# Kernel tuning notes

Hardware: AMD Instinct MI355X
Metric: run time of the kernel (lower is better)

## Reference

```python
import jax, jax.numpy as jnp
import numpy as np

CHANNELS = 256
LAYERS = 4
IN_FEAT = 118
N_NODES = 20000
N_EDGES = 320000


def setup_inputs() -> dict:
    key = jax.random.key(0)
    ks = jax.random.split(key, 4 + 4 * LAYERS)
    x = jax.random.normal(ks[0], (N_NODES, IN_FEAT), dtype=jnp.float32)
    edge_index = jax.random.randint(ks[1], (2, N_EDGES), 0, N_NODES, dtype=jnp.int64)
    s = 1.0 / np.sqrt(CHANNELS)
    W_embed = jax.random.normal(ks[2], (IN_FEAT, CHANNELS), dtype=jnp.float32) / np.sqrt(IN_FEAT)
    b_embed = jnp.zeros((CHANNELS,), dtype=jnp.float32)
    W1 = jax.random.normal(ks[3], (LAYERS, CHANNELS, CHANNELS), dtype=jnp.float32) * s
    b1 = jnp.zeros((LAYERS, CHANNELS), dtype=jnp.float32)
    W2 = jax.random.normal(ks[4], (LAYERS, CHANNELS, CHANNELS), dtype=jnp.float32) * s
    b2 = jnp.zeros((LAYERS, CHANNELS), dtype=jnp.float32)
    return {"x": x, "edge_index": edge_index, "W_embed": W_embed, "b_embed": b_embed,
            "W1": W1, "b1": b1, "W2": W2, "b2": b2}


def reference(x, edge_index, W_embed, b_embed, W1, b1, W2, b2):
    n = x.shape[0]
    src, dst = edge_index[0], edge_index[1]
    # in-degree for mean aggregation (constant across layers)
    cnt = jax.ops.segment_sum(jnp.ones(src.shape[0], dtype=x.dtype), dst, num_segments=n)
    inv_cnt = (1.0 / jnp.maximum(cnt, 1.0))[:, None]
    h = x @ W_embed + b_embed  # [N, C]
    for l in range(W1.shape[0]):
        # message: gather source features, dense + exact GELU (dropout off in eval)
        msg = jax.nn.gelu(h[src] @ W1[l] + b1[l], approximate=False)  # [E, C]
        # mean-scatter aggregate over destination nodes
        agg = jax.ops.segment_sum(msg, dst, num_segments=n) * inv_cnt  # [N, C]
        # update: dense + GELU
        h = jax.nn.gelu(agg @ W2[l] + b2[l], approximate=False)
    return jnp.mean(h, axis=1)  # [N]
```

## Files before the change

### kernel.cpp

```cpp
#include <hip/hip_runtime.h>
#include <math.h>

#define CH 256

typedef _Float16 half8 __attribute__((ext_vector_type(8)));
typedef _Float16 half4 __attribute__((ext_vector_type(4)));
typedef float f32x4 __attribute__((ext_vector_type(4)));

__device__ __forceinline__ float gelu_exact(float v) {
    return 0.5f * v * (1.0f + erff(v * 0.70710678118654752f));
}

__global__ void wsplit_kernel(const float* __restrict__ W1, const float* __restrict__ W2,
                              _Float16* __restrict__ WThi, _Float16* __restrict__ WTlo) {
    int idx = blockIdx.x * blockDim.x + threadIdx.x;
    int n   = idx & 255;
    int kg  = (idx >> 8) & 31;
    int mat = idx >> 13;
    const float* W = (mat < 4) ? (W1 + (size_t)mat * 65536)
                               : (W2 + (size_t)(mat - 4) * 65536);
    _Float16 hi[8], lo[8];
#pragma unroll
    for (int j = 0; j < 8; j++) {
        float v = W[(size_t)(kg * 8 + j) * CH + n];
        _Float16 h = (_Float16)v;
        hi[j] = h;
        lo[j] = (_Float16)(v - (float)h);
    }
    size_t off = (size_t)mat * 65536 + (size_t)n * 256 + kg * 8;
    *(half8*)(WThi + off) = *(half8*)&hi[0];
    *(half8*)(WTlo + off) = *(half8*)&lo[0];
}

__global__ void wesplit_kernel(const float* __restrict__ We,
                               _Float16* __restrict__ WeTh, _Float16* __restrict__ WeTl) {
    int idx = blockIdx.x * blockDim.x + threadIdx.x;
    if (idx >= 4096) return;
    int n  = idx >> 4;
    int k8 = (idx & 15) * 8;
    _Float16 hi[8], lo[8];
#pragma unroll
    for (int j = 0; j < 8; j++) {
        int k = k8 + j;
        float v = (k < 118) ? We[(size_t)k * CH + n] : 0.f;
        _Float16 h = (_Float16)v;
        hi[j] = h;
        lo[j] = (_Float16)(v - (float)h);
    }
    size_t off = (size_t)n * 128 + k8;
    *(half8*)(WeTh + off) = *(half8*)&hi[0];
    *(half8*)(WeTl + off) = *(half8*)&lo[0];
}

__global__ void xsplit_kernel(const float* __restrict__ x,
                              _Float16* __restrict__ xh, _Float16* __restrict__ xl, int N) {
    int idx = blockIdx.x * blockDim.x + threadIdx.x;
    int n  = idx >> 4;
    int c8 = (idx & 15) * 8;
    if (n >= N) return;
    _Float16 hi[8], lo[8];
#pragma unroll
    for (int j = 0; j < 8; j++) {
        int c = c8 + j;
        float v = (c < 118) ? x[(size_t)n * 118 + c] : 0.f;
        _Float16 h = (_Float16)v;
        hi[j] = h;
        lo[j] = (_Float16)(v - (float)h);
    }
    size_t off = (size_t)n * 128 + c8;
    *(half8*)(xh + off) = *(half8*)&hi[0];
    *(half8*)(xl + off) = *(half8*)&lo[0];
}

template<int KT, bool DOGELU>
__global__ __launch_bounds__(256, 4) void mgemm_kernel(
    const _Float16* __restrict__ Ah_g, const _Float16* __restrict__ Al_g,
    const _Float16* __restrict__ Bh_g, const _Float16* __restrict__ Bl_g,
    const float* __restrict__ bias,
    _Float16* __restrict__ Oh, _Float16* __restrict__ Ol,
    int M)
{
    const int KLEN = KT * 32;
    __shared__ _Float16 Ah[128][40], Al[128][40], Bh[64][40], Bl[64][40];

    int tid  = threadIdx.x;
    int lane = tid & 63;
    int wave = tid >> 6;
    int wr = wave >> 1;
    int wc = wave & 1;
    int m0 = blockIdx.x * 128;
    int n0 = blockIdx.y * 64;

    f32x4 acc[4][2];
#pragma unroll
    for (int i = 0; i < 4; i++)
#pragma unroll
        for (int j = 0; j < 2; j++) acc[i][j] = (f32x4){0.f, 0.f, 0.f, 0.f};

    const int s_row = tid >> 1;
    const int s_ch  = (tid & 1) * 16;
    const size_t s_arow = (size_t)min(m0 + s_row, M - 1);
    const int bcol = (tid & 127) >> 1;
    const int bch  = (tid & 1) * 16;

    for (int kt = 0; kt < KT; kt++) {
        int k0 = kt * 32;
        {
            const _Float16* sh_ = Ah_g + s_arow * KLEN + k0 + s_ch;
            const _Float16* sl_ = Al_g + s_arow * KLEN + k0 + s_ch;
            half8 h0 = ((const half8*)sh_)[0];
            half8 h1 = ((const half8*)sh_)[1];
            half8 l0 = ((const half8*)sl_)[0];
            half8 l1 = ((const half8*)sl_)[1];
            *(half8*)&Ah[s_row][s_ch]     = h0;
            *(half8*)&Ah[s_row][s_ch + 8] = h1;
            *(half8*)&Al[s_row][s_ch]     = l0;
            *(half8*)&Al[s_row][s_ch + 8] = l1;
        }
        {
            const _Float16* bs = ((tid < 128) ? Bh_g : Bl_g)
                                 + (size_t)(n0 + bcol) * KLEN + k0 + bch;
            half8 u0 = ((const half8*)bs)[0];
            half8 u1 = ((const half8*)bs)[1];
            _Float16 (*dst)[40] = (tid < 128) ? Bh : Bl;
            *(half8*)&dst[bcol][bch]     = u0;
            *(half8*)&dst[bcol][bch + 8] = u1;
        }
        __syncthreads();

        {
            int frow = lane & 15;
            int fk   = (lane >> 4) * 8;
            half8 ah[4], al[4], bh[2], bl[2];
#pragma unroll
            for (int rf = 0; rf < 4; rf++) {
                int r = wr * 64 + rf * 16 + frow;
                ah[rf] = *(const half8*)&Ah[r][fk];
                al[rf] = *(const half8*)&Al[r][fk];
            }
#pragma unroll
            for (int cf = 0; cf < 2; cf++) {
                int c = wc * 32 + cf * 16 + frow;
                bh[cf] = *(const half8*)&Bh[c][fk];
                bl[cf] = *(const half8*)&Bl[c][fk];
            }
#pragma unroll
            for (int rf = 0; rf < 4; rf++)
#pragma unroll
                for (int cf = 0; cf < 2; cf++) {
                    acc[rf][cf] = __builtin_amdgcn_mfma_f32_16x16x32_f16(ah[rf], bh[cf], acc[rf][cf], 0, 0, 0);
                    acc[rf][cf] = __builtin_amdgcn_mfma_f32_16x16x32_f16(ah[rf], bl[cf], acc[rf][cf], 0, 0, 0);
                    acc[rf][cf] = __builtin_amdgcn_mfma_f32_16x16x32_f16(al[rf], bh[cf], acc[rf][cf], 0, 0, 0);
                }
        }
        __syncthreads();
    }

    int ccol = lane & 15;
    int crow = (lane >> 4) * 4;
#pragma unroll
    for (int cf = 0; cf < 2; cf++) {
        int gcol = n0 + wc * 32 + cf * 16 + ccol;
        float bb = bias[gcol];
#pragma unroll
        for (int rf = 0; rf < 4; rf++) {
#pragma unroll
            for (int q = 0; q < 4; q++) {
                int grow = m0 + wr * 64 + rf * 16 + crow + q;
                if (grow < M) {
                    float v = acc[rf][cf][q] + bb;
                    float g = DOGELU ? gelu_exact(v) : v;
                    _Float16 hi = (_Float16)g;
                    Oh[(size_t)grow * CH + gcol] = hi;
                    Ol[(size_t)grow * CH + gcol] = (_Float16)(g - (float)hi);
                }
            }
        }
    }
}

__global__ void zero_int_kernel(int* p, int n) {
    int i = blockIdx.x * blockDim.x + threadIdx.x;
    if (i < n) p[i] = 0;
}

__global__ void degree_kernel(const int* __restrict__ ei, int E, int* deg) {
    int e = blockIdx.x * blockDim.x + threadIdx.x;
    if (e < E) atomicAdd(&deg[ei[E + e]], 1);
}

__global__ void scan_part_kernel(const int* __restrict__ deg, int* bsum, int N) {
    int t = threadIdx.x;
    int base = blockIdx.x * 1024 + t * 4;
    int4 v = {0, 0, 0, 0};
    if (base + 3 < N) v = *(const int4*)(deg + base);
    else {
        if (base + 0 < N) v.x = deg[base + 0];
        if (base + 1 < N) v.y = deg[base + 1];
        if (base + 2 < N) v.z = deg[base + 2];
        if (base + 3 < N) v.w = deg[base + 3];
    }
    __shared__ int sh[256];
    sh[t] = v.x + v.y + v.z + v.w;
    __syncthreads();
    for (int off = 128; off; off >>= 1) {
        if (t < off) sh[t] += sh[t + off];
        __syncthreads();
    }
    if (t == 0) bsum[blockIdx.x] = sh[0];
}

__global__ void scan_top_kernel(const int* __restrict__ bsum, int* boff, int B) {
    __shared__ int sh[256];
    int t = threadIdx.x;
    int own = (t < B) ? bsum[t] : 0;
    sh[t] = own;
    __syncthreads();
    for (int off = 1; off < 256; off <<= 1) {
        int v = (t >= off) ? sh[t - off] : 0;
        __syncthreads();
        sh[t] += v;
        __syncthreads();
    }
    if (t < B) boff[t] = sh[t] - own;
}

__global__ void scan_final_kernel(const int* __restrict__ deg, const int* __restrict__ boff,
                                  int* row_ptr, int* fill_pos, float* inv, int N, int E) {
    int t = threadIdx.x;
    int base = blockIdx.x * 1024 + t * 4;
    int4 v = {0, 0, 0, 0};
    if (base + 3 < N) v = *(const int4*)(deg + base);
    else {
        if (base + 0 < N) v.x = deg[base + 0];
        if (base + 1 < N) v.y = deg[base + 1];
        if (base + 2 < N) v.z = deg[base + 2];
        if (base + 3 < N) v.w = deg[base + 3];
    }
    int own = v.x + v.y + v.z + v.w;
    __shared__ int sh[256];
    sh[t] = own;
    __syncthreads();
    for (int off = 1; off < 256; off <<= 1) {
        int s = (t >= off) ? sh[t - off] : 0;
        __syncthreads();
        sh[t] += s;
        __syncthreads();
    }
    int run = boff[blockIdx.x] + (sh[t] - own);
    int4 rp;
    rp.x = run;
    rp.y = run + v.x;
    rp.z = rp.y + v.y;
    rp.w = rp.z + v.z;
    if (base + 3 < N) {
        *(int4*)(row_ptr + base) = rp;
        *(int4*)(fill_pos + base) = rp;
        float4 iv;
        iv.x = 1.0f / fmaxf((float)v.x, 1.0f);
        iv.y = 1.0f / fmaxf((float)v.y, 1.0f);
        iv.z = 1.0f / fmaxf((float)v.z, 1.0f);
        iv.w = 1.0f / fmaxf((float)v.w, 1.0f);
        *(float4*)(inv + base) = iv;
    } else {
        int rr[4] = {rp.x, rp.y, rp.z, rp.w};
        int dd[4] = {v.x, v.y, v.z, v.w};
        for (int q = 0; q < 4; q++) {
            if (base + q < N) {
                row_ptr[base + q] = rr[q];
                fill_pos[base + q] = rr[q];
                inv[base + q] = 1.0f / fmaxf((float)dd[q], 1.0f);
            }
        }
    }
    if (blockIdx.x == 0 && t == 0) row_ptr[N] = E;
}

__global__ void fill_kernel(const int* __restrict__ ei, int E, int* fill_pos, int* colv) {
    int e = blockIdx.x * blockDim.x + threadIdx.x;
    if (e < E) {
        int p = atomicAdd(&fill_pos[ei[E + e]], 1);
        colv[p] = ei[e];
    }
}

__global__ void agg_kernel(const _Float16* __restrict__ th, const _Float16* __restrict__ tl,
                           const int* __restrict__ row_ptr, const int* __restrict__ colv,
                           const float* __restrict__ inv,
                           _Float16* __restrict__ aggh, _Float16* __restrict__ aggl, int N) {
    int n = blockIdx.x * 4 + (threadIdx.x >> 6);
    if (n >= N) return;
    int lane = threadIdx.x & 63;
    int s = row_ptr[n], e = row_ptr[n + 1];
    size_t loff = (size_t)lane * 4;

    f32x4 a0 = {0.f, 0.f, 0.f, 0.f}, a1 = a0, a2 = a0, a3 = a0;
    int j = s;
    for (; j + 4 <= e; j += 4) {
        int c0 = colv[j], c1 = colv[j + 1], c2 = colv[j + 2], c3 = colv[j + 3];
        half4 h0 = *(const half4*)(th + (size_t)c0 * CH + loff);
        half4 l0 = *(const half4*)(tl + (size_t)c0 * CH + loff);
        half4 h1 = *(const half4*)(th + (size_t)c1 * CH + loff);
        half4 l1 = *(const half4*)(tl + (size_t)c1 * CH + loff);
        half4 h2 = *(const half4*)(th + (size_t)c2 * CH + loff);
        half4 l2 = *(const half4*)(tl + (size_t)c2 * CH + loff);
        half4 h3 = *(const half4*)(th + (size_t)c3 * CH + loff);
        half4 l3 = *(const half4*)(tl + (size_t)c3 * CH + loff);
#pragma unroll
        for (int q = 0; q < 4; q++) {
            a0[q] += (float)h0[q] + (float)l0[q];
            a1[q] += (float)h1[q] + (float)l1[q];
            a2[q] += (float)h2[q] + (float)l2[q];
            a3[q] += (float)h3[q] + (float)l3[q];
        }
    }
    for (; j < e; j++) {
        int c = colv[j];
        half4 h = *(const half4*)(th + (size_t)c * CH + loff);
        half4 l = *(const half4*)(tl + (size_t)c * CH + loff);
#pragma unroll
        for (int q = 0; q < 4; q++) a0[q] += (float)h[q] + (float)l[q];
    }
    f32x4 tot = (a0 + a1) + (a2 + a3);
    float sc = inv[n];
    _Float16 oh[4], ol[4];
#pragma unroll
    for (int q = 0; q < 4; q++) {
        float v = tot[q] * sc;
        _Float16 hi = (_Float16)v;
        oh[q] = hi;
        ol[q] = (_Float16)(v - (float)hi);
    }
    *(half4*)(aggh + (size_t)n * CH + loff) = *(half4*)&oh[0];
    *(half4*)(aggl + (size_t)n * CH + loff) = *(half4*)&ol[0];
}

__global__ void mean_kernel(const _Float16* __restrict__ hh, const _Float16* __restrict__ hl,
                            float* __restrict__ out, int N) {
    int n = blockIdx.x * 4 + (threadIdx.x >> 6);
    if (n >= N) return;
    int lane = threadIdx.x & 63;
    half4 vh = *(const half4*)(hh + (size_t)n * CH + lane * 4);
    half4 vl = *(const half4*)(hl + (size_t)n * CH + lane * 4);
    float s = 0.f;
#pragma unroll
    for (int q = 0; q < 4; q++) s += (float)vh[q] + (float)vl[q];
#pragma unroll
    for (int off = 32; off; off >>= 1) s += __shfl_down(s, off, 64);
    if (lane == 0) out[n] = s * (1.0f / 256.0f);
}

extern "C" void kernel_launch(void* const* d_in, const int* in_sizes, int n_in,
                              void* d_out, int out_size, void* d_ws, size_t ws_size,
                              hipStream_t stream) {
    const float* x       = (const float*)d_in[0];
    const int*   ei      = (const int*)d_in[1];
    const float* W_embed = (const float*)d_in[2];
    const float* b_embed = (const float*)d_in[3];
    const float* W1      = (const float*)d_in[4];
    const float* b1      = (const float*)d_in[5];
    const float* W2      = (const float*)d_in[6];
    const float* b2      = (const float*)d_in[7];
    float* out = (float*)d_out;

    int N = in_sizes[0] / 118;
    int E = in_sizes[1] / 2;
    int SB = (N + 1023) / 1024;
    size_t NC = (size_t)N * CH;

    _Float16* hh   = (_Float16*)d_ws;
    _Float16* hl   = hh + NC;
    _Float16* th   = hl + NC;
    _Float16* tl   = th + NC;
    _Float16* ah   = tl + NC;
    _Float16* al   = ah + NC;
    _Float16* WThi = al + NC;
    _Float16* WTlo = WThi + 8 * 65536;
    _Float16* WeTh = WTlo + 8 * 65536;
    _Float16* WeTl = WeTh + 256 * 128;
    float*    inv      = (float*)(WeTl + 256 * 128);
    int*      deg      = (int*)(inv + N);
    int*      row_ptr  = deg + N;
    int*      fill_pos = row_ptr + (N + 1);
    int*      colv     = fill_pos + N;
    int*      bsum     = colv + E;
    int*      boff     = bsum + 256;

    _Float16* xh = th;
    _Float16* xl = th + (size_t)N * 128;

    zero_int_kernel<<<(N + 255) / 256, 256, 0, stream>>>(deg, N);
    degree_kernel<<<(E + 255) / 256, 256, 0, stream>>>(ei, E, deg);
    scan_part_kernel<<<SB, 256, 0, stream>>>(deg, bsum, N);
    scan_top_kernel<<<1, 256, 0, stream>>>(bsum, boff, SB);
    scan_final_kernel<<<SB, 256, 0, stream>>>(deg, boff, row_ptr, fill_pos, inv, N, E);
    fill_kernel<<<(E + 255) / 256, 256, 0, stream>>>(ei, E, fill_pos, colv);
    wsplit_kernel<<<256, 256, 0, stream>>>(W1, W2, WThi, WTlo);
    wesplit_kernel<<<16, 256, 0, stream>>>(W_embed, WeTh, WeTl);
    xsplit_kernel<<<(N * 16 + 255) / 256, 256, 0, stream>>>(x, xh, xl, N);

    dim3 mg((N + 127) / 128, 4);
    mgemm_kernel<4, false><<<mg, 256, 0, stream>>>(xh, xl, WeTh, WeTl, b_embed, hh, hl, N);

    for (int l = 0; l < 4; l++) {
        mgemm_kernel<8, true><<<mg, 256, 0, stream>>>(hh, hl,
                                                      WThi + (size_t)l * 65536,
                                                      WTlo + (size_t)l * 65536,
                                                      b1 + (size_t)l * CH, th, tl, N);
        agg_kernel<<<(N + 3) / 4, 256, 0, stream>>>(th, tl, row_ptr, colv, inv, ah, al, N);
        mgemm_kernel<8, true><<<mg, 256, 0, stream>>>(ah, al,
                                                      WThi + (size_t)(4 + l) * 65536,
                                                      WTlo + (size_t)(4 + l) * 65536,
                                                      b2 + (size_t)l * CH, hh, hl, N);
    }
    mean_kernel<<<(N + 3) / 4, 256, 0, stream>>>(hh, hl, out, N);
}
```

Before: 482.7 us.

## Retile split-fp16 GEMM to full-width 64x256 blocks and deepen aggregation unroll

The GEMM block now covers 64 rows by all 256 output columns with 512 threads (8 waves), so each A tile is loaded once per row block rather than re-read by four column blocks. Each block stages a larger B tile in LDS. The aggregation kernel's gather loop is unrolled from 4 to 8 neighbours to keep more loads in flight. The trade-offs are more LDS per block and fewer blocks (313), which may lower occupancy and leave the GPU's compute units less evenly loaded.

```diff
diff --git a/kernel.cpp b/kernel.cpp
--- a/kernel.cpp
+++ b/kernel.cpp
@@ -73,7 +73,7 @@
 }
 
 template<int KT, bool DOGELU>
-__global__ __launch_bounds__(256, 4) void mgemm_kernel(
+__global__ __launch_bounds__(512, 4) void mgemm_kernel(
     const _Float16* __restrict__ Ah_g, const _Float16* __restrict__ Al_g,
     const _Float16* __restrict__ Bh_g, const _Float16* __restrict__ Bl_g,
     const float* __restrict__ bias,
@@ -81,73 +81,71 @@
     int M)
 {
     const int KLEN = KT * 32;
-    __shared__ _Float16 Ah[128][40], Al[128][40], Bh[64][40], Bl[64][40];
+    __shared__ _Float16 Ah[64][40], Al[64][40], Bh[256][40], Bl[256][40];
 
     int tid  = threadIdx.x;
     int lane = tid & 63;
     int wave = tid >> 6;
-    int wr = wave >> 1;
-    int wc = wave & 1;
-    int m0 = blockIdx.x * 128;
-    int n0 = blockIdx.y * 64;
-
-    f32x4 acc[4][2];
-#pragma unroll
-    for (int i = 0; i < 4; i++)
-#pragma unroll
-        for (int j = 0; j < 2; j++) acc[i][j] = (f32x4){0.f, 0.f, 0.f, 0.f};
-
-    const int s_row = tid >> 1;
-    const int s_ch  = (tid & 1) * 16;
-    const size_t s_arow = (size_t)min(m0 + s_row, M - 1);
-    const int bcol = (tid & 127) >> 1;
-    const int bch  = (tid & 1) * 16;
+    int wr = wave >> 2;
+    int wc = wave & 3;
+    int m0 = blockIdx.x * 64;
+
+    f32x4 acc[2][4];
+#pragma unroll
+    for (int i = 0; i < 2; i++)
+#pragma unroll
+        for (int j = 0; j < 4; j++) acc[i][j] = (f32x4){0.f, 0.f, 0.f, 0.f};
+
+    const int a_row = tid >> 3;
+    const int a_sel = tid & 7;
+    const int a_arr = a_sel >> 2;
+    const int a_ch  = (a_sel & 3) * 8;
+    const size_t a_grow = (size_t)min(m0 + a_row, M - 1);
+    const int b_col = tid & 255;
+    const int b_ch  = (tid >> 8) * 16;
 
     for (int kt = 0; kt < KT; kt++) {
         int k0 = kt * 32;
         {
-            const _Float16* sh_ = Ah_g + s_arow * KLEN + k0 + s_ch;
-            const _Float16* sl_ = Al_g + s_arow * KLEN + k0 + s_ch;
+            const _Float16* src = (a_arr ? Al_g : Ah_g) + a_grow * KLEN + k0 + a_ch;
+            half8 v = *(const half8*)src;
+            if (a_arr) *(half8*)&Al[a_row][a_ch] = v;
+            else       *(half8*)&Ah[a_row][a_ch] = v;
+        }
+        {
+            const _Float16* sh_ = Bh_g + (size_t)b_col * KLEN + k0 + b_ch;
+            const _Float16* sl_ = Bl_g + (size_t)b_col * KLEN + k0 + b_ch;
             half8 h0 = ((const half8*)sh_)[0];
             half8 h1 = ((const half8*)sh_)[1];
             half8 l0 = ((const half8*)sl_)[0];
             half8 l1 = ((const half8*)sl_)[1];
-            *(half8*)&Ah[s_row][s_ch]     = h0;
-            *(half8*)&Ah[s_row][s_ch + 8] = h1;
-            *(half8*)&Al[s_row][s_ch]     = l0;
-            *(half8*)&Al[s_row][s_ch + 8] = l1;
-        }
-        {
-            const _Float16* bs = ((tid < 128) ? Bh_g : Bl_g)
-                                 + (size_t)(n0 + bcol) * KLEN + k0 + bch;
-            half8 u0 = ((const half8*)bs)[0];
-            half8 u1 = ((const half8*)bs)[1];
-            _Float16 (*dst)[40] = (tid < 128) ? Bh : Bl;
-            *(half8*)&dst[bcol][bch]     = u0;
-            *(half8*)&dst[bcol][bch + 8] = u1;
+            *(half8*)&Bh[b_col][b_ch]     = h0;
+            *(half8*)&Bh[b_col][b_ch + 8] = h1;
+            *(half8*)&Bl[b_col][b_ch]     = l0;
+            *(half8*)&Bl[b_col][b_ch + 8] = l1;
         }
         __syncthreads();
 
         {
             int frow = lane & 15;
             int fk   = (lane >> 4) * 8;
-            half8 ah[4], al[4], bh[2], bl[2];
-#pragma unroll
-            for (int rf = 0; rf < 4; rf++) {
-                int r = wr * 64 + rf * 16 + frow;
+            half8 ah[2], al[2], bh[4], bl[4];
+#pragma unroll
+            for (int rf = 0; rf < 2; rf++) {
+                int r = wr * 32 + rf * 16 + frow;
                 ah[rf] = *(const half8*)&Ah[r][fk];
                 al[rf] = *(const half8*)&Al[r][fk];
             }
 #pragma unroll
-            for (int cf = 0; cf < 2; cf++) {
-                int c = wc * 32 + cf * 16 + frow;
+            for (int cf = 0; cf < 4; cf++) {
+                int c = wc * 64 + cf * 16 + frow;
                 bh[cf] = *(const half8*)&Bh[c][fk];
                 bl[cf] = *(const half8*)&Bl[c][fk];
             }
 #pragma unroll
-            for (int rf = 0; rf < 4; rf++)
-#pragma unroll
-                for (int cf = 0; cf < 2; cf++) {
+            for (int rf = 0; rf < 2; rf++)
+#pragma unroll
+                for (int cf = 0; cf < 4; cf++) {
                     acc[rf][cf] = __builtin_amdgcn_mfma_f32_16x16x32_f16(ah[rf], bh[cf], acc[rf][cf], 0, 0, 0);
                     acc[rf][cf] = __builtin_amdgcn_mfma_f32_16x16x32_f16(ah[rf], bl[cf], acc[rf][cf], 0, 0, 0);
                     acc[rf][cf] = __builtin_amdgcn_mfma_f32_16x16x32_f16(al[rf], bh[cf], acc[rf][cf], 0, 0, 0);
@@ -159,14 +157,14 @@
     int ccol = lane & 15;
     int crow = (lane >> 4) * 4;
 #pragma unroll
-    for (int cf = 0; cf < 2; cf++) {
-        int gcol = n0 + wc * 32 + cf * 16 + ccol;
+    for (int cf = 0; cf < 4; cf++) {
+        int gcol = wc * 64 + cf * 16 + ccol;
         float bb = bias[gcol];
 #pragma unroll
-        for (int rf = 0; rf < 4; rf++) {
+        for (int rf = 0; rf < 2; rf++) {
 #pragma unroll
             for (int q = 0; q < 4; q++) {
-                int grow = m0 + wr * 64 + rf * 16 + crow + q;
+                int grow = m0 + wr * 32 + rf * 16 + crow + q;
                 if (grow < M) {
                     float v = acc[rf][cf][q] + bb;
                     float g = DOGELU ? gelu_exact(v) : v;
@@ -296,22 +294,22 @@
 
     f32x4 a0 = {0.f, 0.f, 0.f, 0.f}, a1 = a0, a2 = a0, a3 = a0;
     int j = s;
-    for (; j + 4 <= e; j += 4) {
-        int c0 = colv[j], c1 = colv[j + 1], c2 = colv[j + 2], c3 = colv[j + 3];
-        half4 h0 = *(const half4*)(th + (size_t)c0 * CH + loff);
-        half4 l0 = *(const half4*)(tl + (size_t)c0 * CH + loff);
-        half4 h1 = *(const half4*)(th + (size_t)c1 * CH + loff);
-        half4 l1 = *(const half4*)(tl + (size_t)c1 * CH + loff);
-        half4 h2 = *(const half4*)(th + (size_t)c2 * CH + loff);
-        half4 l2 = *(const half4*)(tl + (size_t)c2 * CH + loff);
-        half4 h3 = *(const half4*)(th + (size_t)c3 * CH + loff);
-        half4 l3 = *(const half4*)(tl + (size_t)c3 * CH + loff);
+    for (; j + 8 <= e; j += 8) {
+        int c[8];
+#pragma unroll
+        for (int u = 0; u < 8; u++) c[u] = colv[j + u];
+        half4 hv[8], lv[8];
+#pragma unroll
+        for (int u = 0; u < 8; u++) {
+            hv[u] = *(const half4*)(th + (size_t)c[u] * CH + loff);
+            lv[u] = *(const half4*)(tl + (size_t)c[u] * CH + loff);
+        }
 #pragma unroll
         for (int q = 0; q < 4; q++) {
-            a0[q] += (float)h0[q] + (float)l0[q];
-            a1[q] += (float)h1[q] + (float)l1[q];
-            a2[q] += (float)h2[q] + (float)l2[q];
-            a3[q] += (float)h3[q] + (float)l3[q];
+            a0[q] += (float)hv[0][q] + (float)lv[0][q] + (float)hv[4][q] + (float)lv[4][q];
+            a1[q] += (float)hv[1][q] + (float)lv[1][q] + (float)hv[5][q] + (float)lv[5][q];
+            a2[q] += (float)hv[2][q] + (float)lv[2][q] + (float)hv[6][q] + (float)lv[6][q];
+            a3[q] += (float)hv[3][q] + (float)lv[3][q] + (float)hv[7][q] + (float)lv[7][q];
         }
     }
     for (; j < e; j++) {
@@ -399,16 +397,16 @@
     wesplit_kernel<<<16, 256, 0, stream>>>(W_embed, WeTh, WeTl);
     xsplit_kernel<<<(N * 16 + 255) / 256, 256, 0, stream>>>(x, xh, xl, N);
 
-    dim3 mg((N + 127) / 128, 4);
-    mgemm_kernel<4, false><<<mg, 256, 0, stream>>>(xh, xl, WeTh, WeTl, b_embed, hh, hl, N);
+    int mb = (N + 63) / 64;
+    mgemm_kernel<4, false><<<mb, 512, 0, stream>>>(xh, xl, WeTh, WeTl, b_embed, hh, hl, N);
 
     for (int l = 0; l < 4; l++) {
-        mgemm_kernel<8, true><<<mg, 256, 0, stream>>>(hh, hl,
+        mgemm_kernel<8, true><<<mb, 512, 0, stream>>>(hh, hl,
                                                       WThi + (size_t)l * 65536,
                                                       WTlo + (size_t)l * 65536,
                                                       b1 + (size_t)l * CH, th, tl, N);
         agg_kernel<<<(N + 3) / 4, 256, 0, stream>>>(th, tl, row_ptr, colv, inv, ah, al, N);
-        mgemm_kernel<8, true><<<mg, 256, 0, stream>>>(ah, al,
+        mgemm_kernel<8, true><<<mb, 512, 0, stream>>>(ah, al,
                                                       WThi + (size_t)(4 + l) * 65536,
                                                       WTlo + (size_t)(4 + l) * 65536,
                                                       b2 + (size_t)l * CH, hh, hl, N);
```

New measurement: 513.2 us. 6.3% more time.
